# Performance work log

Hardware: AMD Instinct MI355X
Metric: run time of the kernel (lower is better)

Reference implementation:

```python
import jax, jax.numpy as jnp
import numpy as np

N_FEATS = 512
SND = N_FEATS // 2
N_NODES = 100000
NUM_GRAPHS = 256
EPS = 1e-5


def graph_norm(x, batch, num_seg, w, b, ms):
    # PyG GraphNorm: out = w * (x - mean[batch]*mean_scale) / sqrt(var[batch]+eps) + b
    cnt = jax.ops.segment_sum(jnp.ones((x.shape[0],), x.dtype), batch, num_seg)
    cnt = jnp.maximum(cnt, 1.0)[:, None]
    mean = jax.ops.segment_sum(x, batch, num_seg) / cnt
    sub = x - mean[batch] * ms
    var = jax.ops.segment_sum(sub * sub, batch, num_seg) / cnt
    return w * sub * jax.lax.rsqrt(var[batch] + EPS) + b


def graph_norm_global(x, w, b, ms):
    # gn3 is called without `batch` in the source -> batch=None -> global stats
    mean = jnp.mean(x, axis=0, keepdims=True)
    sub = x - mean * ms
    var = jnp.mean(sub * sub, axis=0, keepdims=True)
    return w * sub * jax.lax.rsqrt(var + EPS) + b


def prelu(x, a):
    return jnp.where(x >= 0, x, a * x)


def linear(x, W, b):
    return x @ W.T + b


def setup_inputs() -> dict:
    key = jax.random.key(0)
    ks = jax.random.split(key, 12)
    d = {}
    d['x'] = jax.random.normal(ks[0], (N_NODES, N_FEATS), jnp.float32)
    d['batch'] = jnp.sort(jax.random.randint(ks[1], (N_NODES,), 0, NUM_GRAPHS)).astype(jnp.int64)
    # GraphNorm params (PyG init: weight=1, bias=0, mean_scale=1)
    for name, dim in [('gn1', N_FEATS), ('gn2', SND), ('gn3', SND), ('gn4', SND), ('gn5', SND)]:
        d[name + '_w'] = jnp.ones((dim,), jnp.float32)
        d[name + '_b'] = jnp.zeros((dim,), jnp.float32)
        d[name + '_ms'] = jnp.ones((dim,), jnp.float32)
    # Linear weights/biases
    d['lin1_W'] = jax.random.normal(ks[2], (SND, N_FEATS), jnp.float32) * 0.02
    d['lin1_b'] = jnp.zeros((SND,), jnp.float32)
    d['lin2_W'] = jax.random.normal(ks[3], (SND, SND), jnp.float32) * 0.02
    d['lin2_b'] = jnp.zeros((SND,), jnp.float32)
    d['lin3_W'] = jax.random.normal(ks[4], (SND, SND), jnp.float32) * 0.02
    d['lin3_b'] = jnp.zeros((SND,), jnp.float32)
    d['lin4_W'] = jax.random.normal(ks[5], (SND, SND), jnp.float32) * 0.02
    d['lin4_b'] = jnp.zeros((SND,), jnp.float32)
    d['lin5_W'] = jax.random.normal(ks[6], (N_FEATS, SND), jnp.float32) * 0.02
    d['lin5_b'] = jnp.zeros((N_FEATS,), jnp.float32)
    # PReLU params (single param, init 0.25)
    for name in ['a2', 'a3', 'a4', 'a5']:
        d[name] = jnp.full((1,), 0.25, jnp.float32)
    return d


def reference(x, batch,
              gn1_w, gn1_b, gn1_ms, gn2_w, gn2_b, gn2_ms, gn3_w, gn3_b, gn3_ms,
              gn4_w, gn4_b, gn4_ms, gn5_w, gn5_b, gn5_ms,
              lin1_W, lin1_b, lin2_W, lin2_b, lin3_W, lin3_b, lin4_W, lin4_b,
              lin5_W, lin5_b, a2, a3, a4, a5):
    # x = lin1(gn1(x, batch))
    x1 = linear(graph_norm(x, batch, NUM_GRAPHS, gn1_w, gn1_b, gn1_ms), lin1_W, lin1_b)
    # x = (lin3(gn3(lin2(gn2(x, batch)))) + x) / 2   [gn3 uses global stats]
    h = linear(prelu(graph_norm(x1, batch, NUM_GRAPHS, gn2_w, gn2_b, gn2_ms), a2), lin2_W, lin2_b)
    h = linear(prelu(graph_norm_global(h, gn3_w, gn3_b, gn3_ms), a3), lin3_W, lin3_b)
    x2 = (h + x1) / 2
    # x = (lin4(gn4(x, batch)) + x) / 2
    h = linear(prelu(graph_norm(x2, batch, NUM_GRAPHS, gn4_w, gn4_b, gn4_ms), a4), lin4_W, lin4_b)
    x3 = (h + x2) / 2
    # x = lin5(gn5(x, batch))
    out = linear(prelu(graph_norm(x3, batch, NUM_GRAPHS, gn5_w, gn5_b, gn5_ms), a5), lin5_W, lin5_b)
    return out
```

## Files before the change

### kernel.cpp

```cpp
#include <hip/hip_runtime.h>
#include <cstddef>
#include <cstdint>

#define NF 512
#define SND 256
#define NG 256
#define EPSV 1e-5f

typedef __attribute__((ext_vector_type(8))) short bf16x8;
typedef __attribute__((ext_vector_type(4))) float f32x4;

__device__ __forceinline__ float bf2f(unsigned short u) {
  return __uint_as_float(((unsigned int)u) << 16);
}
__device__ __forceinline__ unsigned short f2bf(float f) {
  unsigned int u = __float_as_uint(f);
  return (unsigned short)((u + 0x7fffu + ((u >> 16) & 1u)) >> 16);
}
__device__ __forceinline__ unsigned int pack2bf(float a, float b) {
  return (unsigned int)f2bf(a) | ((unsigned int)f2bf(b) << 16);
}

__device__ __forceinline__ void async16(const unsigned short* g, unsigned short* l) {
  __builtin_amdgcn_global_load_lds(
      (const __attribute__((address_space(1))) unsigned int*)g,
      (__attribute__((address_space(3))) unsigned int*)l, 16, 0, 0);
}

__global__ void offsets_kernel(const int* __restrict__ batch, int* __restrict__ offs, int M) {
  int t = threadIdx.x + blockIdx.x * blockDim.x;
  if (t > NG) return;
  if (t == NG) { offs[NG] = M; return; }
  int lo = 0, hi = M;
  while (lo < hi) { int mid = (lo + hi) >> 1; if (batch[mid] < t) lo = mid + 1; else hi = mid; }
  offs[t] = lo;
}

__global__ void wconv_kernel(const float* __restrict__ w1, const float* __restrict__ w2,
                             const float* __restrict__ w3, const float* __restrict__ w4,
                             const float* __restrict__ w5,
                             unsigned short* __restrict__ o1, unsigned short* __restrict__ o2,
                             unsigned short* __restrict__ o3, unsigned short* __restrict__ o4,
                             unsigned short* __restrict__ o5) {
  int i = threadIdx.x + blockIdx.x * 256;
  if (i < 131072) { o1[i] = f2bf(w1[i]); o5[i] = f2bf(w5[i]); }
  if (i < 65536)  { o2[i] = f2bf(w2[i]); o3[i] = f2bf(w3[i]); o4[i] = f2bf(w4[i]); }
}

template <typename T, int F, int VE, bool WB, bool GLOB>
__global__ void stats_k(const T* __restrict__ X, const int* __restrict__ offs, int M,
                        float* __restrict__ ps, float* __restrict__ pq,
                        unsigned short* __restrict__ xbf) {
  constexpr int TPR = F / VE, RPB = 256 / TPR;
  const int g = GLOB ? 0 : blockIdx.x;
  const int s = GLOB ? 0 : offs[g];
  const int e = GLOB ? M : offs[g + 1];
  const int slot = threadIdx.x / TPR;
  const int f0 = (threadIdx.x % TPR) * VE;
  float a0[VE], a1[VE];
#pragma unroll
  for (int i = 0; i < VE; ++i) { a0[i] = 0.f; a1[i] = 0.f; }

  for (int r = s + (int)blockIdx.y * RPB + slot; r < e; r += (int)gridDim.y * RPB) {
    float v[VE];
    if constexpr (sizeof(T) == 2) {
      const uint4 u = *(const uint4*)((const unsigned short*)X + (size_t)r * F + f0);
      v[0] = __uint_as_float(u.x << 16); v[1] = __uint_as_float(u.x & 0xffff0000u);
      v[2] = __uint_as_float(u.y << 16); v[3] = __uint_as_float(u.y & 0xffff0000u);
      v[4] = __uint_as_float(u.z << 16); v[5] = __uint_as_float(u.z & 0xffff0000u);
      v[6] = __uint_as_float(u.w << 16); v[7] = __uint_as_float(u.w & 0xffff0000u);
    } else {
      const float4 u = *(const float4*)((const float*)X + (size_t)r * F + f0);
      v[0] = u.x; v[1] = u.y; v[2] = u.z; v[3] = u.w;
    }
#pragma unroll
    for (int i = 0; i < VE; ++i) { a0[i] += v[i]; a1[i] += v[i] * v[i]; }
    if constexpr (WB) {
      *(uint2*)(xbf + (size_t)r * F + f0) = make_uint2(pack2bf(v[0], v[1]), pack2bf(v[2], v[3]));
    }
  }

  const int groups = GLOB ? 1 : (int)gridDim.x;
  const size_t pbase = (size_t)blockIdx.y * ((size_t)groups * F) + (size_t)g * F + f0;

  __shared__ float red[256 * VE];
  __syncthreads();
#pragma unroll
  for (int i = 0; i < VE; ++i) red[slot * F + f0 + i] = a0[i];
  __syncthreads();
  if (slot == 0) {
    float t[VE];
#pragma unroll
    for (int i = 0; i < VE; ++i) {
      t[i] = 0.f;
      for (int sl = 0; sl < RPB; ++sl) t[i] += red[sl * F + f0 + i];
    }
#pragma unroll
    for (int i = 0; i < VE; i += 4)
      *(float4*)&ps[pbase + i] = make_float4(t[i], t[i + 1], t[i + 2], t[i + 3]);
  }
  __syncthreads();
#pragma unroll
  for (int i = 0; i < VE; ++i) red[slot * F + f0 + i] = a1[i];
  __syncthreads();
  if (slot == 0) {
    float t[VE];
#pragma unroll
    for (int i = 0; i < VE; ++i) {
      t[i] = 0.f;
      for (int sl = 0; sl < RPB; ++sl) t[i] += red[sl * F + f0 + i];
    }
#pragma unroll
    for (int i = 0; i < VE; i += 4)
      *(float4*)&pq[pbase + i] = make_float4(t[i], t[i + 1], t[i + 2], t[i + 3]);
  }
}

__global__ void finalize_kernel(const float* __restrict__ ps, const float* __restrict__ pq,
                                const float* __restrict__ w, const float* __restrict__ b,
                                const float* __restrict__ ms, const int* __restrict__ offs,
                                int F, int P,
                                float* __restrict__ sc, float* __restrict__ sh) {
  int idx = threadIdx.x + blockIdx.x * 256;
  int g = idx / F, f = idx - g * F;
  int total = (int)gridDim.x * 256;
  float s0 = 0.f, s1 = 0.f;
  for (int p = 0; p < P; ++p) {
    s0 += ps[(size_t)p * total + idx];
    s1 += pq[(size_t)p * total + idx];
  }
  float cnt = fmaxf((float)(offs[g + 1] - offs[g]), 1.0f);
  float mean = s0 / cnt;
  float ex2  = s1 / cnt;
  float mm = mean * ms[f];
  float var = ex2 - 2.f * mm * mean + mm * mm;
  float rstd = rsqrtf(var + EPSV);
  float s = w[f] * rstd;
  sc[idx] = s;
  sh[idx] = b[f] - mm * s;
}

__global__ void finalize_glob_kernel(const float* __restrict__ ps, const float* __restrict__ pq,
                                     const float* __restrict__ w, const float* __restrict__ b,
                                     const float* __restrict__ ms, int cnt_i, int F, int P,
                                     float* __restrict__ sc, float* __restrict__ sh) {
  const int fl = threadIdx.x & 15;
  const int pl = threadIdx.x >> 4;
  const int f = blockIdx.x * 16 + fl;
  float s0 = 0.f, s1 = 0.f;
  for (int p = pl; p < P; p += 16) {
    s0 += ps[(size_t)p * F + f];
    s1 += pq[(size_t)p * F + f];
  }
  __shared__ float r0[16][16], r1[16][16];
  r0[pl][fl] = s0;
  r1[pl][fl] = s1;
  __syncthreads();
  if (pl == 0) {
#pragma unroll
    for (int k = 1; k < 16; ++k) { s0 += r0[k][fl]; s1 += r1[k][fl]; }
    float cnt = fmaxf((float)cnt_i, 1.0f);
    float mean = s0 / cnt;
    float ex2  = s1 / cnt;
    float mm = mean * ms[f];
    float var = ex2 - 2.f * mm * mean + mm * mm;
    float rstd = rsqrtf(var + EPSV);
    float s = w[f] * rstd;
    sc[f] = s;
    sh[f] = b[f] - mm * s;
  }
}

template <int K, bool PRELU, bool GLOB>
__global__ void norm_act(const unsigned short* __restrict__ Xin, unsigned short* __restrict__ Aout,
                         const float* __restrict__ SC, const float* __restrict__ SH,
                         const int* __restrict__ batch, const float* __restrict__ pa, int M) {
  constexpr int TPR = K / 8, RPB = 256 / TPR;
  const int row = blockIdx.x * RPB + threadIdx.x / TPR;
  if (row >= M) return;
  const int f0 = (threadIdx.x % TPR) * 8;
  const int g = GLOB ? 0 : batch[row];
  const float a = PRELU ? pa[0] : 0.f;
  const uint4 u = *(const uint4*)(Xin + (size_t)row * K + f0);
  const float4 s0 = *(const float4*)(SC + (size_t)g * K + f0);
  const float4 s1 = *(const float4*)(SC + (size_t)g * K + f0 + 4);
  const float4 h0 = *(const float4*)(SH + (size_t)g * K + f0);
  const float4 h1 = *(const float4*)(SH + (size_t)g * K + f0 + 4);
  float v[8];
  v[0] = __uint_as_float(u.x << 16); v[1] = __uint_as_float(u.x & 0xffff0000u);
  v[2] = __uint_as_float(u.y << 16); v[3] = __uint_as_float(u.y & 0xffff0000u);
  v[4] = __uint_as_float(u.z << 16); v[5] = __uint_as_float(u.z & 0xffff0000u);
  v[6] = __uint_as_float(u.w << 16); v[7] = __uint_as_float(u.w & 0xffff0000u);
  v[0] = fmaf(v[0], s0.x, h0.x); v[1] = fmaf(v[1], s0.y, h0.y);
  v[2] = fmaf(v[2], s0.z, h0.z); v[3] = fmaf(v[3], s0.w, h0.w);
  v[4] = fmaf(v[4], s1.x, h1.x); v[5] = fmaf(v[5], s1.y, h1.y);
  v[6] = fmaf(v[6], s1.z, h1.z); v[7] = fmaf(v[7], s1.w, h1.w);
  if (PRELU) {
#pragma unroll
    for (int i = 0; i < 8; ++i) v[i] = v[i] >= 0.f ? v[i] : a * v[i];
  }
  *(uint4*)(Aout + (size_t)row * K + f0) =
      make_uint4(pack2bf(v[0], v[1]), pack2bf(v[2], v[3]),
                 pack2bf(v[4], v[5]), pack2bf(v[6], v[7]));
}

template <int K, bool RESID, bool OUT_BF>
__global__ __launch_bounds__(256, 4)
void gemm_bf16(const unsigned short* __restrict__ A, const unsigned short* __restrict__ Bw,
               const float* __restrict__ lb_, const unsigned short* __restrict__ resid,
               void* __restrict__ outv, int M, int N) {
  __shared__ __align__(16) unsigned short sA[128 * 64];
  __shared__ __align__(16) unsigned short sB[128 * 64];
  const int tid = threadIdx.x;
  const int wave = tid >> 6, lane = tid & 63;
  const int m0 = blockIdx.y * 128, n0 = blockIdx.x * 128;
  const int wm = wave & 1, wn = wave >> 1;
  const int qd = lane >> 4, l15 = lane & 15;

  const int srow = lane >> 3;
  const int schunk = lane & 7;
  const int gchunk = schunk ^ srow;

  f32x4 acc[4][4];
#pragma unroll
  for (int mi = 0; mi < 4; ++mi)
#pragma unroll
    for (int ni = 0; ni < 4; ++ni) acc[mi][ni] = (f32x4){0.f, 0.f, 0.f, 0.f};

  const unsigned short* Abase = A + (size_t)m0 * K;
  const unsigned short* Bbase = Bw + (size_t)n0 * K;

  for (int kt = 0; kt < K / 64; ++kt) {
    const int kOff = kt * 64 + gchunk * 8;
#pragma unroll
    for (int i = 0; i < 4; ++i) {
      const int r = wave * 32 + i * 8 + srow;
      async16(Abase + (size_t)r * K + kOff, &sA[(wave * 4 + i) * 512]);
      async16(Bbase + (size_t)r * K + kOff, &sB[(wave * 4 + i) * 512]);
    }
    __syncthreads();
#pragma unroll
    for (int ks = 0; ks < 2; ++ks) {
      bf16x8 af[4], bfr[4];
      const int pc = ((ks * 4 + qd) ^ (l15 & 7)) * 8;
#pragma unroll
      for (int mi = 0; mi < 4; ++mi)
        af[mi] = *(const bf16x8*)&sA[(wm * 64 + mi * 16 + l15) * 64 + pc];
#pragma unroll
      for (int ni = 0; ni < 4; ++ni)
        bfr[ni] = *(const bf16x8*)&sB[(wn * 64 + ni * 16 + l15) * 64 + pc];
#pragma unroll
      for (int mi = 0; mi < 4; ++mi)
#pragma unroll
        for (int ni = 0; ni < 4; ++ni)
          acc[mi][ni] = __builtin_amdgcn_mfma_f32_16x16x32_bf16(af[mi], bfr[ni], acc[mi][ni], 0, 0, 0);
    }
    __syncthreads();
  }

  float lb[4];
#pragma unroll
  for (int ni = 0; ni < 4; ++ni) lb[ni] = lb_[n0 + wn * 64 + ni * 16 + l15];
  float* outF = (float*)outv;
  unsigned short* outH = (unsigned short*)outv;
#pragma unroll
  for (int mi = 0; mi < 4; ++mi) {
#pragma unroll
    for (int i = 0; i < 4; ++i) {
      const int row = m0 + wm * 64 + mi * 16 + qd * 4 + i;
      if (row >= M) continue;
#pragma unroll
      for (int ni = 0; ni < 4; ++ni) {
        const int col = n0 + wn * 64 + ni * 16 + l15;
        float v = acc[mi][ni][i] + lb[ni];
        if (RESID) v = 0.5f * (v + bf2f(resid[(size_t)row * N + col]));
        if (OUT_BF) outH[(size_t)row * N + col] = f2bf(v);
        else        outF[(size_t)row * N + col] = v;
      }
    }
  }
}

extern "C" void kernel_launch(void* const* d_in, const int* in_sizes, int n_in,
                              void* d_out, int out_size, void* d_ws, size_t ws_size,
                              hipStream_t stream) {
  const float* x    = (const float*)d_in[0];
  const int* batch  = (const int*)d_in[1];
  const float* gw1 = (const float*)d_in[2],  *gb1 = (const float*)d_in[3],  *gm1 = (const float*)d_in[4];
  const float* gw2 = (const float*)d_in[5],  *gb2 = (const float*)d_in[6],  *gm2 = (const float*)d_in[7];
  const float* gw3 = (const float*)d_in[8],  *gb3 = (const float*)d_in[9],  *gm3 = (const float*)d_in[10];
  const float* gw4 = (const float*)d_in[11], *gb4 = (const float*)d_in[12], *gm4 = (const float*)d_in[13];
  const float* gw5 = (const float*)d_in[14], *gb5 = (const float*)d_in[15], *gm5 = (const float*)d_in[16];
  const float* W1 = (const float*)d_in[17], *b1 = (const float*)d_in[18];
  const float* W2 = (const float*)d_in[19], *b2 = (const float*)d_in[20];
  const float* W3 = (const float*)d_in[21], *b3 = (const float*)d_in[22];
  const float* W4 = (const float*)d_in[23], *b4 = (const float*)d_in[24];
  const float* W5 = (const float*)d_in[25], *b5 = (const float*)d_in[26];
  const float* a2 = (const float*)d_in[27], *a3 = (const float*)d_in[28];
  const float* a4 = (const float*)d_in[29], *a5 = (const float*)d_in[30];
  float* out = (float*)d_out;
  (void)n_in; (void)out_size; (void)ws_size;

  const int M = in_sizes[0] / NF;
  const int MT = (M + 127) / 128;
  const int M_pad = MT * 128;

  char* wsp = (char*)d_ws;
  size_t off = 0;
  auto take = [&](size_t bytes) -> void* {
    void* p = wsp + off;
    off = (off + bytes + 255) & ~(size_t)255;
    return p;
  };
  int* offs            = (int*)take((NG + 1) * sizeof(int));
  unsigned short* Wb1  = (unsigned short*)take((size_t)SND * NF * 2);
  unsigned short* Wb2  = (unsigned short*)take((size_t)SND * SND * 2);
  unsigned short* Wb3  = (unsigned short*)take((size_t)SND * SND * 2);
  unsigned short* Wb4  = (unsigned short*)take((size_t)SND * SND * 2);
  unsigned short* Wb5  = (unsigned short*)take((size_t)NF * SND * 2);
  float* psum          = (float*)take((size_t)8 * NG * NF * 4);
  float* psq           = (float*)take((size_t)8 * NG * NF * 4);
  float* sc            = (float*)take((size_t)NG * NF * 4);
  float* sh            = (float*)take((size_t)NG * NF * 4);
  unsigned short* B1   = (unsigned short*)take((size_t)M_pad * SND * 2);
  unsigned short* B2   = (unsigned short*)take((size_t)M_pad * SND * 2);
  unsigned short* Abuf = (unsigned short*)take((size_t)M_pad * NF * 2);

  offsets_kernel<<<2, 256, 0, stream>>>(batch, offs, M);
  wconv_kernel<<<512, 256, 0, stream>>>(W1, W2, W3, W4, W5, Wb1, Wb2, Wb3, Wb4, Wb5);

  stats_k<float, NF, 4, true, false><<<dim3(NG, 8), 256, 0, stream>>>(x, offs, M, psum, psq, Abuf);
  finalize_kernel<<<(NG * NF) / 256, 256, 0, stream>>>(psum, psq, gw1, gb1, gm1, offs, NF, 8, sc, sh);
  norm_act<NF, false, false><<<(M + 3) / 4, 256, 0, stream>>>(Abuf, Abuf, sc, sh, batch, nullptr, M);
  gemm_bf16<NF, false, true><<<dim3(SND / 128, MT), 256, 0, stream>>>(Abuf, Wb1, b1, nullptr, B1, M, SND);

  stats_k<unsigned short, SND, 8, false, false><<<dim3(NG, 4), 256, 0, stream>>>(B1, offs, M, psum, psq, nullptr);
  finalize_kernel<<<(NG * SND) / 256, 256, 0, stream>>>(psum, psq, gw2, gb2, gm2, offs, SND, 4, sc, sh);
  norm_act<SND, true, false><<<(M + 7) / 8, 256, 0, stream>>>(B1, Abuf, sc, sh, batch, a2, M);
  gemm_bf16<SND, false, true><<<dim3(SND / 128, MT), 256, 0, stream>>>(Abuf, Wb2, b2, nullptr, B2, M, SND);

  stats_k<unsigned short, SND, 8, false, true><<<dim3(1, 512), 256, 0, stream>>>(B2, offs, M, psum, psq, nullptr);
  finalize_glob_kernel<<<SND / 16, 256, 0, stream>>>(psum, psq, gw3, gb3, gm3, M, SND, 512, sc, sh);
  norm_act<SND, true, true><<<(M + 7) / 8, 256, 0, stream>>>(B2, Abuf, sc, sh, nullptr, a3, M);
  gemm_bf16<SND, true, true><<<dim3(SND / 128, MT), 256, 0, stream>>>(Abuf, Wb3, b3, B1, B2, M, SND);

  stats_k<unsigned short, SND, 8, false, false><<<dim3(NG, 4), 256, 0, stream>>>(B2, offs, M, psum, psq, nullptr);
  finalize_kernel<<<(NG * SND) / 256, 256, 0, stream>>>(psum, psq, gw4, gb4, gm4, offs, SND, 4, sc, sh);
  norm_act<SND, true, false><<<(M + 7) / 8, 256, 0, stream>>>(B2, Abuf, sc, sh, batch, a4, M);
  gemm_bf16<SND, true, true><<<dim3(SND / 128, MT), 256, 0, stream>>>(Abuf, Wb4, b4, B2, B1, M, SND);

  stats_k<unsigned short, SND, 8, false, false><<<dim3(NG, 4), 256, 0, stream>>>(B1, offs, M, psum, psq, nullptr);
  finalize_kernel<<<(NG * SND) / 256, 256, 0, stream>>>(psum, psq, gw5, gb5, gm5, offs, SND, 4, sc, sh);
  norm_act<SND, true, false><<<(M + 7) / 8, 256, 0, stream>>>(B1, Abuf, sc, sh, batch, a5, M);
  gemm_bf16<SND, false, false><<<dim3(NF / 128, MT), 256, 0, stream>>>(Abuf, Wb5, b5, nullptr, out, M, NF);
}
```

Before: 796.7 us.

## Fuse GraphNorm scale/shift and PReLU into GEMM A-tile loading

Removes the separate norm_act kernels by applying per-graph scale/shift and PReLU while loading A tiles into shared memory inside the GEMM, replacing the async global-to-LDS load for A with register loads, conversion and LDS stores. This drops one full read and write of the activation matrix per layer. In exchange, the A loads are no longer asynchronous, the per-row scale/shift loads are repeated for each N-tile block, and launch bounds drop to 3 blocks per SM to allow for higher register use. Buffer assignments for the residual layers are rearranged to avoid aliasing between input and output.

```diff
diff --git a/kernel.cpp b/kernel.cpp
--- a/kernel.cpp
+++ b/kernel.cpp
@@ -19,6 +19,12 @@
 }
 __device__ __forceinline__ unsigned int pack2bf(float a, float b) {
   return (unsigned int)f2bf(a) | ((unsigned int)f2bf(b) << 16);
+}
+__device__ __forceinline__ void unpack8(const uint4 u, float* v) {
+  v[0] = __uint_as_float(u.x << 16); v[1] = __uint_as_float(u.x & 0xffff0000u);
+  v[2] = __uint_as_float(u.y << 16); v[3] = __uint_as_float(u.y & 0xffff0000u);
+  v[4] = __uint_as_float(u.z << 16); v[5] = __uint_as_float(u.z & 0xffff0000u);
+  v[6] = __uint_as_float(u.w << 16); v[7] = __uint_as_float(u.w & 0xffff0000u);
 }
 
 __device__ __forceinline__ void async16(const unsigned short* g, unsigned short* l) {
@@ -65,10 +71,7 @@
     float v[VE];
     if constexpr (sizeof(T) == 2) {
       const uint4 u = *(const uint4*)((const unsigned short*)X + (size_t)r * F + f0);
-      v[0] = __uint_as_float(u.x << 16); v[1] = __uint_as_float(u.x & 0xffff0000u);
-      v[2] = __uint_as_float(u.y << 16); v[3] = __uint_as_float(u.y & 0xffff0000u);
-      v[4] = __uint_as_float(u.z << 16); v[5] = __uint_as_float(u.z & 0xffff0000u);
-      v[6] = __uint_as_float(u.w << 16); v[7] = __uint_as_float(u.w & 0xffff0000u);
+      unpack8(u, v);
     } else {
       const float4 u = *(const float4*)((const float*)X + (size_t)r * F + f0);
       v[0] = u.x; v[1] = u.y; v[2] = u.z; v[3] = u.w;
@@ -171,44 +174,14 @@
   }
 }
 
-template <int K, bool PRELU, bool GLOB>
-__global__ void norm_act(const unsigned short* __restrict__ Xin, unsigned short* __restrict__ Aout,
-                         const float* __restrict__ SC, const float* __restrict__ SH,
-                         const int* __restrict__ batch, const float* __restrict__ pa, int M) {
-  constexpr int TPR = K / 8, RPB = 256 / TPR;
-  const int row = blockIdx.x * RPB + threadIdx.x / TPR;
-  if (row >= M) return;
-  const int f0 = (threadIdx.x % TPR) * 8;
-  const int g = GLOB ? 0 : batch[row];
-  const float a = PRELU ? pa[0] : 0.f;
-  const uint4 u = *(const uint4*)(Xin + (size_t)row * K + f0);
-  const float4 s0 = *(const float4*)(SC + (size_t)g * K + f0);
-  const float4 s1 = *(const float4*)(SC + (size_t)g * K + f0 + 4);
-  const float4 h0 = *(const float4*)(SH + (size_t)g * K + f0);
-  const float4 h1 = *(const float4*)(SH + (size_t)g * K + f0 + 4);
-  float v[8];
-  v[0] = __uint_as_float(u.x << 16); v[1] = __uint_as_float(u.x & 0xffff0000u);
-  v[2] = __uint_as_float(u.y << 16); v[3] = __uint_as_float(u.y & 0xffff0000u);
-  v[4] = __uint_as_float(u.z << 16); v[5] = __uint_as_float(u.z & 0xffff0000u);
-  v[6] = __uint_as_float(u.w << 16); v[7] = __uint_as_float(u.w & 0xffff0000u);
-  v[0] = fmaf(v[0], s0.x, h0.x); v[1] = fmaf(v[1], s0.y, h0.y);
-  v[2] = fmaf(v[2], s0.z, h0.z); v[3] = fmaf(v[3], s0.w, h0.w);
-  v[4] = fmaf(v[4], s1.x, h1.x); v[5] = fmaf(v[5], s1.y, h1.y);
-  v[6] = fmaf(v[6], s1.z, h1.z); v[7] = fmaf(v[7], s1.w, h1.w);
-  if (PRELU) {
-#pragma unroll
-    for (int i = 0; i < 8; ++i) v[i] = v[i] >= 0.f ? v[i] : a * v[i];
-  }
-  *(uint4*)(Aout + (size_t)row * K + f0) =
-      make_uint4(pack2bf(v[0], v[1]), pack2bf(v[2], v[3]),
-                 pack2bf(v[4], v[5]), pack2bf(v[6], v[7]));
-}
-
-template <int K, bool RESID, bool OUT_BF>
-__global__ __launch_bounds__(256, 4)
-void gemm_bf16(const unsigned short* __restrict__ A, const unsigned short* __restrict__ Bw,
-               const float* __restrict__ lb_, const unsigned short* __restrict__ resid,
-               void* __restrict__ outv, int M, int N) {
+template <int K, bool PRELU, bool GLOB, bool RESID, bool OUT_BF>
+__global__ __launch_bounds__(256, 3)
+void gemm_gn_bf16(const unsigned short* __restrict__ A, const int* __restrict__ batch,
+                  const float* __restrict__ SC, const float* __restrict__ SH,
+                  const float* __restrict__ pa,
+                  const unsigned short* __restrict__ Bw,
+                  const float* __restrict__ lb_, const unsigned short* __restrict__ resid,
+                  void* __restrict__ outv, int M, int N) {
   __shared__ __align__(16) unsigned short sA[128 * 64];
   __shared__ __align__(16) unsigned short sB[128 * 64];
   const int tid = threadIdx.x;
@@ -221,13 +194,24 @@
   const int schunk = lane & 7;
   const int gchunk = schunk ^ srow;
 
+  const float alpha = PRELU ? pa[0] : 0.f;
+
+  int gidx[4];
+  const unsigned short* arow[4];
+#pragma unroll
+  for (int i = 0; i < 4; ++i) {
+    const int grow = m0 + wave * 32 + i * 8 + srow;
+    const int rc = grow < M ? grow : M - 1;
+    gidx[i] = GLOB ? 0 : batch[rc];
+    arow[i] = A + (size_t)grow * K;
+  }
+
   f32x4 acc[4][4];
 #pragma unroll
   for (int mi = 0; mi < 4; ++mi)
 #pragma unroll
     for (int ni = 0; ni < 4; ++ni) acc[mi][ni] = (f32x4){0.f, 0.f, 0.f, 0.f};
 
-  const unsigned short* Abase = A + (size_t)m0 * K;
   const unsigned short* Bbase = Bw + (size_t)n0 * K;
 
   for (int kt = 0; kt < K / 64; ++kt) {
@@ -235,8 +219,30 @@
 #pragma unroll
     for (int i = 0; i < 4; ++i) {
       const int r = wave * 32 + i * 8 + srow;
-      async16(Abase + (size_t)r * K + kOff, &sA[(wave * 4 + i) * 512]);
       async16(Bbase + (size_t)r * K + kOff, &sB[(wave * 4 + i) * 512]);
+    }
+#pragma unroll
+    for (int i = 0; i < 4; ++i) {
+      const uint4 u = *(const uint4*)(arow[i] + kOff);
+      const float* scp = SC + (size_t)gidx[i] * K + kOff;
+      const float* shp = SH + (size_t)gidx[i] * K + kOff;
+      const float4 c0 = *(const float4*)scp;
+      const float4 c1 = *(const float4*)(scp + 4);
+      const float4 h0 = *(const float4*)shp;
+      const float4 h1 = *(const float4*)(shp + 4);
+      float v[8];
+      unpack8(u, v);
+      v[0] = fmaf(v[0], c0.x, h0.x); v[1] = fmaf(v[1], c0.y, h0.y);
+      v[2] = fmaf(v[2], c0.z, h0.z); v[3] = fmaf(v[3], c0.w, h0.w);
+      v[4] = fmaf(v[4], c1.x, h1.x); v[5] = fmaf(v[5], c1.y, h1.y);
+      v[6] = fmaf(v[6], c1.z, h1.z); v[7] = fmaf(v[7], c1.w, h1.w);
+      if (PRELU) {
+#pragma unroll
+        for (int j = 0; j < 8; ++j) v[j] = v[j] >= 0.f ? v[j] : alpha * v[j];
+      }
+      *(uint4*)&sA[(wave * 4 + i) * 512 + lane * 8] =
+          make_uint4(pack2bf(v[0], v[1]), pack2bf(v[2], v[3]),
+                     pack2bf(v[4], v[5]), pack2bf(v[6], v[7]));
     }
     __syncthreads();
 #pragma unroll
@@ -325,32 +331,33 @@
   unsigned short* B1   = (unsigned short*)take((size_t)M_pad * SND * 2);
   unsigned short* B2   = (unsigned short*)take((size_t)M_pad * SND * 2);
   unsigned short* Abuf = (unsigned short*)take((size_t)M_pad * NF * 2);
+  unsigned short* A3   = Abuf;
 
   offsets_kernel<<<2, 256, 0, stream>>>(batch, offs, M);
   wconv_kernel<<<512, 256, 0, stream>>>(W1, W2, W3, W4, W5, Wb1, Wb2, Wb3, Wb4, Wb5);
 
   stats_k<float, NF, 4, true, false><<<dim3(NG, 8), 256, 0, stream>>>(x, offs, M, psum, psq, Abuf);
   finalize_kernel<<<(NG * NF) / 256, 256, 0, stream>>>(psum, psq, gw1, gb1, gm1, offs, NF, 8, sc, sh);
-  norm_act<NF, false, false><<<(M + 3) / 4, 256, 0, stream>>>(Abuf, Abuf, sc, sh, batch, nullptr, M);
-  gemm_bf16<NF, false, true><<<dim3(SND / 128, MT), 256, 0, stream>>>(Abuf, Wb1, b1, nullptr, B1, M, SND);
+  gemm_gn_bf16<NF, false, false, false, true><<<dim3(SND / 128, MT), 256, 0, stream>>>(
+      Abuf, batch, sc, sh, nullptr, Wb1, b1, nullptr, B1, M, SND);
 
   stats_k<unsigned short, SND, 8, false, false><<<dim3(NG, 4), 256, 0, stream>>>(B1, offs, M, psum, psq, nullptr);
   finalize_kernel<<<(NG * SND) / 256, 256, 0, stream>>>(psum, psq, gw2, gb2, gm2, offs, SND, 4, sc, sh);
-  norm_act<SND, true, false><<<(M + 7) / 8, 256, 0, stream>>>(B1, Abuf, sc, sh, batch, a2, M);
-  gemm_bf16<SND, false, true><<<dim3(SND / 128, MT), 256, 0, stream>>>(Abuf, Wb2, b2, nullptr, B2, M, SND);
+  gemm_gn_bf16<SND, true, false, false, true><<<dim3(SND / 128, MT), 256, 0, stream>>>(
+      B1, batch, sc, sh, a2, Wb2, b2, nullptr, B2, M, SND);
 
   stats_k<unsigned short, SND, 8, false, true><<<dim3(1, 512), 256, 0, stream>>>(B2, offs, M, psum, psq, nullptr);
   finalize_glob_kernel<<<SND / 16, 256, 0, stream>>>(psum, psq, gw3, gb3, gm3, M, SND, 512, sc, sh);
-  norm_act<SND, true, true><<<(M + 7) / 8, 256, 0, stream>>>(B2, Abuf, sc, sh, nullptr, a3, M);
-  gemm_bf16<SND, true, true><<<dim3(SND / 128, MT), 256, 0, stream>>>(Abuf, Wb3, b3, B1, B2, M, SND);
-
-  stats_k<unsigned short, SND, 8, false, false><<<dim3(NG, 4), 256, 0, stream>>>(B2, offs, M, psum, psq, nullptr);
+  gemm_gn_bf16<SND, true, true, true, true><<<dim3(SND / 128, MT), 256, 0, stream>>>(
+      B2, nullptr, sc, sh, a3, Wb3, b3, B1, A3, M, SND);
+
+  stats_k<unsigned short, SND, 8, false, false><<<dim3(NG, 4), 256, 0, stream>>>(A3, offs, M, psum, psq, nullptr);
   finalize_kernel<<<(NG * SND) / 256, 256, 0, stream>>>(psum, psq, gw4, gb4, gm4, offs, SND, 4, sc, sh);
-  norm_act<SND, true, false><<<(M + 7) / 8, 256, 0, stream>>>(B2, Abuf, sc, sh, batch, a4, M);
-  gemm_bf16<SND, true, true><<<dim3(SND / 128, MT), 256, 0, stream>>>(Abuf, Wb4, b4, B2, B1, M, SND);
+  gemm_gn_bf16<SND, true, false, true, true><<<dim3(SND / 128, MT), 256, 0, stream>>>(
+      A3, batch, sc, sh, a4, Wb4, b4, A3, B1, M, SND);
 
   stats_k<unsigned short, SND, 8, false, false><<<dim3(NG, 4), 256, 0, stream>>>(B1, offs, M, psum, psq, nullptr);
   finalize_kernel<<<(NG * SND) / 256, 256, 0, stream>>>(psum, psq, gw5, gb5, gm5, offs, SND, 4, sc, sh);
-  norm_act<SND, true, false><<<(M + 7) / 8, 256, 0, stream>>>(B1, Abuf, sc, sh, batch, a5, M);
-  gemm_bf16<SND, false, false><<<dim3(NF / 128, MT), 256, 0, stream>>>(Abuf, Wb5, b5, nullptr, out, M, NF);
-}
+  gemm_gn_bf16<SND, true, false, false, false><<<dim3(NF / 128, MT), 256, 0, stream>>>(
+      B1, batch, sc, sh, a5, Wb5, b5, nullptr, out, M, NF);
+}
```

Result: no change. 812.6 us (+2.0%).
